# Optimization experiments

Hardware: AMD Instinct MI355X
Metric: run time of the kernel (lower is better)

## Reference

```python
import jax, jax.numpy as jnp
import numpy as np

B, S, D, H = 4, 2048, 256, 8
HD = D // H  # head_dim = 32
SCALING = HD ** -0.5


def setup_inputs() -> dict:
    key = jax.random.key(0)
    ks = jax.random.split(key, 10)
    glorot = jax.nn.initializers.glorot_uniform()
    inp = {
        "hidden_states": jax.random.normal(ks[0], (B, S, D), jnp.float32),
        "position_embeddings": jax.random.normal(ks[1], (B, S, D), jnp.float32),
        "attention_mask": jnp.zeros((B, S, S), jnp.float32),
        # projection params: EinsumDense 'abc,cde->abde' kernels [D, H, HD]
        "Wq": glorot(ks[2], (D, H, HD), jnp.float32),
        "bq": jnp.zeros((H, HD), jnp.float32),
        "Wk": glorot(ks[3], (D, H, HD), jnp.float32),
        "bk": jnp.zeros((H, HD), jnp.float32),
        "Wv": glorot(ks[4], (D, H, HD), jnp.float32),
        "bv": jnp.zeros((H, HD), jnp.float32),
        # out_proj: 'abc,cd->abd' kernel [D, D]
        "Wo": glorot(ks[5], (D, D), jnp.float32),
        "bo": jnp.zeros((D,), jnp.float32),
    }
    return inp


def reference(hidden_states, position_embeddings, attention_mask,
              Wq, bq, Wk, bk, Wv, bv, Wo, bo):
    # Q/K use hidden + pos embeddings; V uses original hidden states
    hp = hidden_states + position_embeddings
    q = jnp.einsum("bsd,dhe->bshe", hp, Wq) + bq            # [B,S,H,HD]
    k = jnp.einsum("bsd,dhe->bshe", hp, Wk) + bk
    v = jnp.einsum("bsd,dhe->bshe", hidden_states, Wv) + bv
    q = q * SCALING
    scores = jnp.einsum("bqhe,bkhe->bhqk", q, k)            # [B,H,S,S]
    scores = scores + attention_mask[:, None, :, :]         # additive mask
    attn = jax.nn.softmax(scores, axis=-1)
    ctx = jnp.einsum("bhqk,bkhe->bqhe", attn, v)            # [B,S,H,HD]
    ctx = ctx.reshape(ctx.shape[0], ctx.shape[1], D)        # [B,S,D]
    out = jnp.einsum("bsd,de->bse", ctx, Wo) + bo
    return out
```

## Files before the change

### kernel.cpp

```cpp
#include <hip/hip_runtime.h>
#include <hip/hip_bf16.h>

#define Bsz 4
#define Ssz 2048
#define Dsz 256
#define Hh 8
#define HDd 32

typedef __attribute__((ext_vector_type(8))) short bh8;
typedef __attribute__((ext_vector_type(4))) float f4;
typedef __attribute__((ext_vector_type(4))) unsigned u4;
typedef __attribute__((ext_vector_type(2))) unsigned u2;

#define SCAL 0.17677669529663687f
#define LOG2E 1.4426950408889634f
#define QSCALE (SCAL * LOG2E)

__device__ __forceinline__ short f2bf(float f) {
    union { float f; unsigned u; } x; x.f = f;
    unsigned r = x.u + 0x7fffu + ((x.u >> 16) & 1u);
    return (short)(r >> 16);
}

__device__ __forceinline__ float bf2f(short s) {
    union { unsigned u; float f; } x;
    x.u = ((unsigned)(unsigned short)s) << 16;
    return x.f;
}

__device__ __forceinline__ float fexp2(float x) {
#if __has_builtin(__builtin_amdgcn_exp2f)
    return __builtin_amdgcn_exp2f(x);
#else
    float r; asm("v_exp_f32 %0, %1" : "=v"(r) : "v"(x)); return r;
#endif
}

__device__ __forceinline__ unsigned cvtpk(float lo, float hi) {
    unsigned r; asm("v_cvt_pk_bf16_f32 %0, %1, %2" : "=v"(r) : "v"(lo), "v"(hi));
    return r;
}

__device__ __forceinline__ void gload16(const void* g, void* l) {
    __builtin_amdgcn_global_load_lds(
        (const __attribute__((address_space(1))) unsigned int*)g,
        (__attribute__((address_space(3))) unsigned int*)l, 16, 0, 0);
}

__global__ __launch_bounds__(256) void prep_fast(
    const float* __restrict__ hid, const float* __restrict__ pos,
    const float* __restrict__ Wq, const float* __restrict__ Wk,
    const float* __restrict__ Wv, const float* __restrict__ Wo,
    const float* __restrict__ bq,
    short* __restrict__ Wf, float* __restrict__ bqs,
    short* __restrict__ hp, short* __restrict__ hv,
    int* __restrict__ flag)
{
    const int bid = blockIdx.x;
    if (bid < 256) {
        int t = bid * 256 + threadIdx.x;
        int d = t >> 8, n = t & 255;
        int off = (((d >> 5) * 16 + (n >> 4)) * 64 + ((d >> 3) & 3) * 16 + (n & 15)) * 8 + (d & 7);
        Wf[off]          = f2bf(Wq[t] * QSCALE);
        Wf[65536 + off]  = f2bf(Wk[t]);
        Wf[131072 + off] = f2bf(Wv[t]);
        Wf[196608 + off] = f2bf(Wo[t]);
        if (t == 0) *flag = 0;
        if (t < 256) bqs[t] = bq[t] * QSCALE;
    } else {
        const size_t i = ((size_t)(bid - 256) * 256 + threadIdx.x) * 8;
        f4 h1 = *(const f4*)(hid + i), h2 = *(const f4*)(hid + i + 4);
        f4 p1 = *(const f4*)(pos + i), p2 = *(const f4*)(pos + i + 4);
        union { unsigned u[4]; bh8 v; } a, b;
        a.u[0] = cvtpk(h1[0] + p1[0], h1[1] + p1[1]);
        a.u[1] = cvtpk(h1[2] + p1[2], h1[3] + p1[3]);
        a.u[2] = cvtpk(h2[0] + p2[0], h2[1] + p2[1]);
        a.u[3] = cvtpk(h2[2] + p2[2], h2[3] + p2[3]);
        b.u[0] = cvtpk(h1[0], h1[1]); b.u[1] = cvtpk(h1[2], h1[3]);
        b.u[2] = cvtpk(h2[0], h2[1]); b.u[3] = cvtpk(h2[2], h2[3]);
        *(bh8*)(hp + i) = a.v;
        *(bh8*)(hv + i) = b.v;
    }
}

__global__ __launch_bounds__(256) void qkv_scan(
    const short* __restrict__ hp, const short* __restrict__ hv,
    const short* __restrict__ Wf, const float* __restrict__ bqs,
    const float* __restrict__ bk, const float* __restrict__ bv,
    const float* __restrict__ mask, int* __restrict__ flag,
    short* __restrict__ Q, short* __restrict__ K, short* __restrict__ Vt)
{
    const int bid = blockIdx.x;
    if (bid >= 1536) {
        const u4* p = (const u4*)mask + (size_t)(bid - 1536) * 4096 + threadIdx.x;
        u4 v[16];
#pragma unroll
        for (int k = 0; k < 16; k++) v[k] = p[(size_t)k * 256];
        const unsigned M = 0x7fffffffu;
        u4 o = (v[0] & M) | (v[1] & M);
#pragma unroll
        for (int k = 2; k < 16; k++) o |= (v[k] & M);
        unsigned a = (o[0] | o[1]) | (o[2] | o[3]);
        if (a != 0u) atomicOr(flag, 1);
        return;
    }
    const int ky = bid >> 9;
    const int w = threadIdx.x >> 6, lane = threadIdx.x & 63;
    const int lg = lane >> 4, lr = lane & 15;
    const int m0 = (bid & 511) * 16;
    const short* A = (ky < 2) ? hp : hv;
    const short* Wb = Wf + ky * 65536 + (w * 4) * 512 + lane * 8;
    f4 acc[4];
#pragma unroll
    for (int t = 0; t < 4; t++) acc[t] = (f4){0.f, 0.f, 0.f, 0.f};

    const short* ap = A + (size_t)(m0 + lr) * 256 + lg * 8;
#pragma unroll
    for (int k0g = 0; k0g < 8; k0g++) {
        bh8 af = *(const bh8*)(ap + k0g * 32);
#pragma unroll
        for (int nt = 0; nt < 4; nt++) {
            bh8 bf = *(const bh8*)(Wb + k0g * 8192 + nt * 512);
            acc[nt] = __builtin_amdgcn_mfma_f32_16x16x32_bf16(af, bf, acc[nt], 0, 0, 0);
        }
    }
    const int b = m0 >> 11;
    const int s0 = m0 & 2047;
#pragma unroll
    for (int nt = 0; nt < 4; nt++) {
        const int n = w * 64 + nt * 16 + lr;
        const int h = n >> 5, hd = n & 31;
#pragma unroll
        for (int r = 0; r < 4; r++) {
            const int s = s0 + lg * 4 + r;
            float v = acc[nt][r];
            if (ky == 0) {
                v += bqs[n];
                Q[(((size_t)(b * Hh + h)) * Ssz + s) * HDd + hd] = f2bf(v);
            } else if (ky == 1) {
                v += bk[n];
                K[(((size_t)(b * Hh + h)) * Ssz + s) * HDd + hd] = f2bf(v);
            } else {
                v += bv[n];
                int s32 = s & 31;
                int ps = ((s32 & 15) >> 2) * 8 + (s32 >> 4) * 4 + (s32 & 3);
                Vt[(((size_t)(b * Hh + h)) * HDd + hd) * Ssz + (s & ~31) + ps] = f2bf(v);
            }
        }
    }
}

template<int NS>
__global__ __launch_bounds__(512) void attn(
    const short* __restrict__ Q, const short* __restrict__ Kb,
    const short* __restrict__ Vt, const float* __restrict__ mask,
    const int* __restrict__ flag, short* __restrict__ ctx,
    short* __restrict__ pacc, float* __restrict__ sums)
{
    __shared__ __align__(16) char lds[24576];
    const int tid = threadIdx.x;
    const int bh = blockIdx.y, b = bh >> 3, h = bh & 7;
    const int w = tid >> 6, lane = tid & 63;
    const int lg = lane >> 4, lr = lane & 15;
    const int q0 = blockIdx.x * 128 + w * 16;
    const int kz0 = blockIdx.z * (Ssz / NS);
    constexpr int NT = Ssz / NS / 64;

    const char* Kg = (const char*)(Kb + (size_t)bh * Ssz * HDd);
    const char* Vg = (const char*)(Vt + (size_t)bh * HDd * Ssz);
    const bool um = (*flag) != 0;
    const float* mrow = mask + ((size_t)b * Ssz + q0 + lr) * Ssz;

    const char* sgp;
    size_t sstep;
    int ldo;
    if (w < 4) {
        const int kt = w * 64 + lane;
        const int kx = (kt * 16) ^ (((kt >> 3) & 3) << 4);
        sgp = Kg + (size_t)kz0 * 64 + kx;
        sstep = 4096;
        ldo = w * 1024;
    } else {
        const int vt2 = (w - 4) * 64 + lane;
        const int vrow = vt2 >> 3;
        const int vcol = ((vt2 & 7) * 16) ^ ((vrow & 7) << 4);
        sgp = Vg + (size_t)vrow * (Ssz * 2) + (size_t)kz0 * 2 + vcol;
        sstep = 128;
        ldo = 4096 + (w - 4) * 1024;
    }

    const int koff  = (lr * 64 + lg * 16) ^ (((lr >> 1) & 3) << 4);
    const int voff0 = 4096 + ((lr * 128 + lg * 16) ^ ((lr & 7) << 4));
    const int voff1 = voff0 ^ 64;

    bh8 qf = *(const bh8*)(Q + ((size_t)bh * Ssz + q0 + lr) * HDd + lg * 8);
    const f4 c8 = {-8.f, -8.f, -8.f, -8.f};
    f4 acc0 = {0.f, 0.f, 0.f, 0.f}, acc1 = {0.f, 0.f, 0.f, 0.f};
    f4 sm = {0.f, 0.f, 0.f, 0.f};
    union { unsigned u[4]; bh8 v; } ones;
#pragma unroll
    for (int j = 0; j < 4; j++) ones.u[j] = 0x3F803F80u;

    auto stage = [&](int t, int buf) {
        gload16(sgp + (size_t)t * sstep, lds + buf * 8192 + ldo);
    };

    auto compute = [&](int t, int bs) {
        const char* kp = lds + bs + koff;
        bh8 k0 = *(const bh8*)(kp);
        bh8 k1 = *(const bh8*)(kp + 1024);
        bh8 k2 = *(const bh8*)(kp + 2048);
        bh8 k3 = *(const bh8*)(kp + 3072);
        const char* vp = lds + bs;
        bh8 v00 = *(const bh8*)(vp + voff0);
        bh8 v01 = *(const bh8*)(vp + voff1);
        bh8 v10 = *(const bh8*)(vp + voff0 + 2048);
        bh8 v11 = *(const bh8*)(vp + voff1 + 2048);

        __builtin_amdgcn_s_setprio(1);
        f4 s0 = __builtin_amdgcn_mfma_f32_16x16x32_bf16(k0, qf, c8, 0, 0, 0);
        f4 s1 = __builtin_amdgcn_mfma_f32_16x16x32_bf16(k1, qf, c8, 0, 0, 0);
        f4 s2 = __builtin_amdgcn_mfma_f32_16x16x32_bf16(k2, qf, c8, 0, 0, 0);
        f4 s3 = __builtin_amdgcn_mfma_f32_16x16x32_bf16(k3, qf, c8, 0, 0, 0);
        __builtin_amdgcn_s_setprio(0);
        if (um) {
            const int kb = kz0 + t * 64;
            f4 m0v = *(const f4*)(mrow + kb + lg * 4);
            f4 m1v = *(const f4*)(mrow + kb + 16 + lg * 4);
            f4 m2v = *(const f4*)(mrow + kb + 32 + lg * 4);
            f4 m3v = *(const f4*)(mrow + kb + 48 + lg * 4);
            s0 += m0v * LOG2E; s1 += m1v * LOG2E; s2 += m2v * LOG2E; s3 += m3v * LOG2E;
        }

        float p[16];
#pragma unroll
        for (int j = 0; j < 4; j++) {
            p[j]      = fexp2(s0[j]);
            p[4 + j]  = fexp2(s1[j]);
            p[8 + j]  = fexp2(s2[j]);
            p[12 + j] = fexp2(s3[j]);
        }
        union { unsigned u[4]; bh8 v; } pf0, pf1;
        pf0.u[0] = cvtpk(p[0], p[1]);   pf0.u[1] = cvtpk(p[2], p[3]);
        pf0.u[2] = cvtpk(p[4], p[5]);   pf0.u[3] = cvtpk(p[6], p[7]);
        pf1.u[0] = cvtpk(p[8], p[9]);   pf1.u[1] = cvtpk(p[10], p[11]);
        pf1.u[2] = cvtpk(p[12], p[13]); pf1.u[3] = cvtpk(p[14], p[15]);

        __builtin_amdgcn_s_setprio(1);
        acc0 = __builtin_amdgcn_mfma_f32_16x16x32_bf16(v00, pf0.v, acc0, 0, 0, 0);
        acc0 = __builtin_amdgcn_mfma_f32_16x16x32_bf16(v01, pf1.v, acc0, 0, 0, 0);
        acc1 = __builtin_amdgcn_mfma_f32_16x16x32_bf16(v10, pf0.v, acc1, 0, 0, 0);
        acc1 = __builtin_amdgcn_mfma_f32_16x16x32_bf16(v11, pf1.v, acc1, 0, 0, 0);
        sm   = __builtin_amdgcn_mfma_f32_16x16x32_bf16(ones.v, pf0.v, sm, 0, 0, 0);
        sm   = __builtin_amdgcn_mfma_f32_16x16x32_bf16(ones.v, pf1.v, sm, 0, 0, 0);
        __builtin_amdgcn_s_setprio(0);
    };

    stage(0, 0);
    stage(1, 1);
    for (int t = 0; t < NT - 1; ++t) {
        asm volatile("s_waitcnt vmcnt(1)" ::: "memory");
        __builtin_amdgcn_s_barrier();
        if (t + 2 < NT) stage(t + 2, (t + 2) % 3);
        compute(t, (t % 3) * 8192);
    }
    asm volatile("s_waitcnt vmcnt(0)" ::: "memory");
    __builtin_amdgcn_s_barrier();
    compute(NT - 1, ((NT - 1) % 3) * 8192);

    const float sum = sm[0];

    if constexpr (NS == 1) {
        float inv = 1.f / sum;
        short* cp = ctx + ((size_t)(b * Ssz + q0 + lr)) * Dsz + h * HDd + lg * 4;
#pragma unroll
        for (int r = 0; r < 4; r++) {
            cp[r]      = f2bf(acc0[r] * inv);
            cp[16 + r] = f2bf(acc1[r] * inv);
        }
    } else {
        const size_t rbase = ((size_t)blockIdx.z * (Bsz * Hh) + bh) * Ssz + q0 + lr;
        short* pa = pacc + rbase * HDd;
        *(u2*)(pa + lg * 4)      = (u2){cvtpk(acc0[0], acc0[1]), cvtpk(acc0[2], acc0[3])};
        *(u2*)(pa + 16 + lg * 4) = (u2){cvtpk(acc1[0], acc1[1]), cvtpk(acc1[2], acc1[3])};
        if (lg == 0) sums[rbase] = sum;
    }
}

template<int SPLIT>
__global__ __launch_bounds__(256) void out_gemm(
    const short* __restrict__ ctx, const short* __restrict__ pacc,
    const float* __restrict__ sums, const short* __restrict__ WfO,
    const float* __restrict__ bo, float* __restrict__ out)
{
    const int w = threadIdx.x >> 6, lane = threadIdx.x & 63;
    const int lg = lane >> 4, lr = lane & 15;
    const int m0 = blockIdx.x * 16;
    const int row = m0 + lr;
    const int b = row >> 11, q = row & 2047;
    f4 acc[4];
#pragma unroll
    for (int t = 0; t < 4; t++) acc[t] = (f4){0.f, 0.f, 0.f, 0.f};
    const short* ap = ctx + (size_t)row * 256 + lg * 8;
    const short* Wb = WfO + (w * 4) * 512 + lane * 8;
    constexpr size_t R = (size_t)(Bsz * Hh) * Ssz;
#pragma unroll
    for (int k0g = 0; k0g < 8; k0g++) {
        const int k0 = k0g * 32;
        union { unsigned u[4]; bh8 v; } af;
        if constexpr (SPLIT) {
            const int h = k0 >> 5;
            const size_t pr = ((size_t)(b * Hh + h)) * Ssz + q;
            const float inv = 1.f / (sums[pr] + sums[R + pr]);
            bh8 x0 = *(const bh8*)(pacc + pr * HDd + lg * 8);
            bh8 x1 = *(const bh8*)(pacc + (R + pr) * HDd + lg * 8);
            af.u[0] = cvtpk((bf2f(x0[0]) + bf2f(x1[0])) * inv, (bf2f(x0[1]) + bf2f(x1[1])) * inv);
            af.u[1] = cvtpk((bf2f(x0[2]) + bf2f(x1[2])) * inv, (bf2f(x0[3]) + bf2f(x1[3])) * inv);
            af.u[2] = cvtpk((bf2f(x0[4]) + bf2f(x1[4])) * inv, (bf2f(x0[5]) + bf2f(x1[5])) * inv);
            af.u[3] = cvtpk((bf2f(x0[6]) + bf2f(x1[6])) * inv, (bf2f(x0[7]) + bf2f(x1[7])) * inv);
        } else {
            af.v = *(const bh8*)(ap + k0);
        }
#pragma unroll
        for (int nt = 0; nt < 4; nt++) {
            bh8 bf = *(const bh8*)(Wb + k0g * 8192 + nt * 512);
            acc[nt] = __builtin_amdgcn_mfma_f32_16x16x32_bf16(af.v, bf, acc[nt], 0, 0, 0);
        }
    }
#pragma unroll
    for (int nt = 0; nt < 4; nt++) {
        const int n = w * 64 + nt * 16 + lr;
        const float bias = bo[n];
#pragma unroll
        for (int r = 0; r < 4; r++) {
            out[(size_t)(m0 + lg * 4 + r) * 256 + n] = acc[nt][r] + bias;
        }
    }
}

extern "C" void kernel_launch(void* const* d_in, const int* in_sizes, int n_in,
                              void* d_out, int out_size, void* d_ws, size_t ws_size,
                              hipStream_t stream)
{
    const float* hid  = (const float*)d_in[0];
    const float* pos  = (const float*)d_in[1];
    const float* mask = (const float*)d_in[2];
    const float* Wq   = (const float*)d_in[3];
    const float* bq   = (const float*)d_in[4];
    const float* Wk   = (const float*)d_in[5];
    const float* bk   = (const float*)d_in[6];
    const float* Wv   = (const float*)d_in[7];
    const float* bv   = (const float*)d_in[8];
    const float* Wo   = (const float*)d_in[9];
    const float* bo   = (const float*)d_in[10];
    float* out = (float*)d_out;

    char* ws = (char*)d_ws;
    short* Wf   = (short*)(ws);
    float* bqs  = (float*)(ws + (512 << 10));
    int*   flag = (int*)  (ws + (516 << 10));
    short* hp   = (short*)(ws + (1  << 20));
    short* hv   = (short*)(ws + (5  << 20));
    short* Qb   = (short*)(ws + (9  << 20));
    short* Kb   = (short*)(ws + (13 << 20));
    short* Vtb  = (short*)(ws + (17 << 20));
    short* ctxb = (short*)(ws + (21 << 20));
    short* pacc = (short*)(ws + (25 << 20));
    float* sums = (float*)(ws + (34 << 20));

    prep_fast<<<1280, 256, 0, stream>>>(hid, pos, Wq, Wk, Wv, Wo, bq, Wf, bqs, hp, hv, flag);
    qkv_scan<<<2560, 256, 0, stream>>>(hp, hv, Wf, bqs, bk, bv, mask, flag, Qb, Kb, Vtb);

    const bool split = ws_size >= ((size_t)36 << 20);
    if (split) {
        attn<2><<<dim3(16, 32, 2), 512, 0, stream>>>(Qb, Kb, Vtb, mask, flag, ctxb, pacc, sums);
        out_gemm<1><<<512, 256, 0, stream>>>(ctxb, pacc, sums, Wf + 196608, bo, out);
    } else {
        attn<1><<<dim3(16, 32, 1), 512, 0, stream>>>(Qb, Kb, Vtb, mask, flag, ctxb, pacc, sums);
        out_gemm<0><<<512, 256, 0, stream>>>(ctxb, pacc, sums, Wf + 196608, bo, out);
    }
}
```

Measured before the change: 74.85 us.

## Fuse Q/K/V projections per block with LDS-staged activations and vectorized stores

Each QKV block now handles 32 rows and all three projections. The hp/hv tiles are staged once into swizzled LDS and reused across Q, K and V, which cuts redundant global activation loads and lowers the block count. MFMA operands are swapped for Q/K and in out_gemm so each lane holds contiguous output columns, allowing packed 8-byte or 16-byte stores instead of scalar ones. The trade-offs are fewer blocks overall and LDS usage that may reduce occupancy.

```diff
diff --git a/kernel.cpp b/kernel.cpp
--- a/kernel.cpp
+++ b/kernel.cpp
@@ -91,8 +91,8 @@
     short* __restrict__ Q, short* __restrict__ K, short* __restrict__ Vt)
 {
     const int bid = blockIdx.x;
-    if (bid >= 1536) {
-        const u4* p = (const u4*)mask + (size_t)(bid - 1536) * 4096 + threadIdx.x;
+    if (bid >= 256) {
+        const u4* p = (const u4*)mask + (size_t)(bid - 256) * 4096 + threadIdx.x;
         u4 v[16];
 #pragma unroll
         for (int k = 0; k < 16; k++) v[k] = p[(size_t)k * 256];
@@ -104,47 +104,71 @@
         if (a != 0u) atomicOr(flag, 1);
         return;
     }
-    const int ky = bid >> 9;
-    const int w = threadIdx.x >> 6, lane = threadIdx.x & 63;
+    __shared__ __align__(16) char lds[32768];
+    const int tid = threadIdx.x;
+    const int w = tid >> 6, lane = tid & 63;
     const int lg = lane >> 4, lr = lane & 15;
-    const int m0 = (bid & 511) * 16;
-    const short* A = (ky < 2) ? hp : hv;
-    const short* Wb = Wf + ky * 65536 + (w * 4) * 512 + lane * 8;
-    f4 acc[4];
-#pragma unroll
-    for (int t = 0; t < 4; t++) acc[t] = (f4){0.f, 0.f, 0.f, 0.f};
-
-    const short* ap = A + (size_t)(m0 + lr) * 256 + lg * 8;
-#pragma unroll
-    for (int k0g = 0; k0g < 8; k0g++) {
-        bh8 af = *(const bh8*)(ap + k0g * 32);
-#pragma unroll
-        for (int nt = 0; nt < 4; nt++) {
-            bh8 bf = *(const bh8*)(Wb + k0g * 8192 + nt * 512);
-            acc[nt] = __builtin_amdgcn_mfma_f32_16x16x32_bf16(af, bf, acc[nt], 0, 0, 0);
-        }
-    }
-    const int b = m0 >> 11;
-    const int s0 = m0 & 2047;
-#pragma unroll
-    for (int nt = 0; nt < 4; nt++) {
-        const int n = w * 64 + nt * 16 + lr;
-        const int h = n >> 5, hd = n & 31;
-#pragma unroll
-        for (int r = 0; r < 4; r++) {
-            const int s = s0 + lg * 4 + r;
-            float v = acc[nt][r];
-            if (ky == 0) {
-                v += bqs[n];
-                Q[(((size_t)(b * Hh + h)) * Ssz + s) * HDd + hd] = f2bf(v);
-            } else if (ky == 1) {
-                v += bk[n];
-                K[(((size_t)(b * Hh + h)) * Ssz + s) * HDd + hd] = f2bf(v);
+    const int m0 = bid * 32;
+    const int b = m0 >> 11, s0 = m0 & 2047;
+
+    const char* hpg = (const char*)(hp + (size_t)m0 * 256);
+    const char* hvg = (const char*)(hv + (size_t)m0 * 256);
+#pragma unroll
+    for (int i = 0; i < 4; i++) {
+        const int L = i * 4096 + tid * 16;
+        const int Ls = L ^ (((L >> 9) & 7) << 4);
+        gload16(hpg + Ls, lds + L);
+        gload16(hvg + Ls, lds + 16384 + L);
+    }
+    asm volatile("s_waitcnt vmcnt(0)" ::: "memory");
+    __builtin_amdgcn_s_barrier();
+
+#pragma unroll
+    for (int ky = 0; ky < 3; ky++) {
+        const char* Al = lds + (ky < 2 ? 0 : 16384);
+        const short* Wb = Wf + ky * 65536 + (w * 4) * 512 + lane * 8;
+#pragma unroll
+        for (int half = 0; half < 2; half++) {
+            f4 acc[4];
+#pragma unroll
+            for (int t = 0; t < 4; t++) acc[t] = (f4){0.f, 0.f, 0.f, 0.f};
+#pragma unroll
+            for (int k0g = 0; k0g < 8; k0g++) {
+                bh8 af = *(const bh8*)(Al +
+                    ((((half * 16 + lr) * 512) + k0g * 64 + lg * 16) ^ ((lr & 7) << 4)));
+#pragma unroll
+                for (int nt = 0; nt < 4; nt++) {
+                    bh8 bf = *(const bh8*)(Wb + k0g * 8192 + nt * 512);
+                    if (ky < 2)
+                        acc[nt] = __builtin_amdgcn_mfma_f32_16x16x32_bf16(bf, af, acc[nt], 0, 0, 0);
+                    else
+                        acc[nt] = __builtin_amdgcn_mfma_f32_16x16x32_bf16(af, bf, acc[nt], 0, 0, 0);
+                }
+            }
+            if (ky < 2) {
+                short* P = (ky == 0) ? Q : K;
+                const float* bb = (ky == 0) ? bqs : bk;
+                const int s = s0 + half * 16 + lr;
+#pragma unroll
+                for (int nt = 0; nt < 4; nt++) {
+                    const int nb = w * 64 + nt * 16 + lg * 4;
+                    const int h = nb >> 5, hd = nb & 31;
+                    f4 bias = *(const f4*)(bb + nb);
+                    u2 o = { cvtpk(acc[nt][0] + bias[0], acc[nt][1] + bias[1]),
+                             cvtpk(acc[nt][2] + bias[2], acc[nt][3] + bias[3]) };
+                    *(u2*)(P + ((size_t)(b * Hh + h) * Ssz + s) * HDd + hd) = o;
+                }
             } else {
-                v += bv[n];
-                int s32 = s & 31;
-                int ps = ((s32 & 15) >> 2) * 8 + (s32 >> 4) * 4 + (s32 & 3);
-                Vt[(((size_t)(b * Hh + h)) * HDd + hd) * Ssz + (s & ~31) + ps] = f2bf(v);
+#pragma unroll
+                for (int nt = 0; nt < 4; nt++) {
+                    const int n = w * 64 + nt * 16 + lr;
+                    const int h = n >> 5, hd = n & 31;
+                    const float bias = bv[n];
+                    u2 o = { cvtpk(acc[nt][0] + bias, acc[nt][1] + bias),
+                             cvtpk(acc[nt][2] + bias, acc[nt][3] + bias) };
+                    *(u2*)(Vt + ((size_t)(b * Hh + h) * HDd + hd) * Ssz
+                               + s0 + lg * 8 + half * 4) = o;
+                }
             }
         }
     }
@@ -306,10 +330,9 @@
     constexpr size_t R = (size_t)(Bsz * Hh) * Ssz;
 #pragma unroll
     for (int k0g = 0; k0g < 8; k0g++) {
-        const int k0 = k0g * 32;
         union { unsigned u[4]; bh8 v; } af;
         if constexpr (SPLIT) {
-            const int h = k0 >> 5;
+            const int h = k0g;
             const size_t pr = ((size_t)(b * Hh + h)) * Ssz + q;
             const float inv = 1.f / (sums[pr] + sums[R + pr]);
             bh8 x0 = *(const bh8*)(pacc + pr * HDd + lg * 8);
@@ -319,22 +342,20 @@
             af.u[2] = cvtpk((bf2f(x0[4]) + bf2f(x1[4])) * inv, (bf2f(x0[5]) + bf2f(x1[5])) * inv);
             af.u[3] = cvtpk((bf2f(x0[6]) + bf2f(x1[6])) * inv, (bf2f(x0[7]) + bf2f(x1[7])) * inv);
         } else {
-            af.v = *(const bh8*)(ap + k0);
+            af.v = *(const bh8*)(ap + k0g * 32);
         }
 #pragma unroll
         for (int nt = 0; nt < 4; nt++) {
             bh8 bf = *(const bh8*)(Wb + k0g * 8192 + nt * 512);
-            acc[nt] = __builtin_amdgcn_mfma_f32_16x16x32_bf16(af.v, bf, acc[nt], 0, 0, 0);
+            acc[nt] = __builtin_amdgcn_mfma_f32_16x16x32_bf16(bf, af.v, acc[nt], 0, 0, 0);
         }
     }
 #pragma unroll
     for (int nt = 0; nt < 4; nt++) {
-        const int n = w * 64 + nt * 16 + lr;
-        const float bias = bo[n];
-#pragma unroll
-        for (int r = 0; r < 4; r++) {
-            out[(size_t)(m0 + lg * 4 + r) * 256 + n] = acc[nt][r] + bias;
-        }
+        const int nb = w * 64 + nt * 16 + lg * 4;
+        f4 bias = *(const f4*)(bo + nb);
+        f4 res = acc[nt] + bias;
+        *(f4*)(out + (size_t)row * 256 + nb) = res;
     }
 }
 
@@ -369,7 +390,7 @@
     float* sums = (float*)(ws + (34 << 20));
 
     prep_fast<<<1280, 256, 0, stream>>>(hid, pos, Wq, Wk, Wv, Wo, bq, Wf, bqs, hp, hv, flag);
-    qkv_scan<<<2560, 256, 0, stream>>>(hp, hv, Wf, bqs, bk, bv, mask, flag, Qb, Kb, Vtb);
+    qkv_scan<<<1280, 256, 0, stream>>>(hp, hv, Wf, bqs, bk, bv, mask, flag, Qb, Kb, Vtb);
 
     const bool split = ws_size >= ((size_t)36 << 20);
     if (split) {
```

After: 96.25 us. 28.6% more time.
